# Kernel optimization log

Hardware: AMD Instinct MI355X
Metric: run time of the kernel (lower is better)

Reference implementation:

```python
import jax, jax.numpy as jnp
import numpy as np
import math

B, T, L, HID, BB, FF, H = 4, 1024, 1024, 1024, 512, 4096, 8
EPS = 1e-6


def _ln(x, g, b):
    m = jnp.mean(x, -1, keepdims=True)
    v = jnp.mean((x - m) ** 2, -1, keepdims=True)
    return (x - m) / jnp.sqrt(v + EPS) * g + b


def _gelu(x):
    # custom tanh-approx GELU from the source
    return 0.5 * x * (1 + jnp.tanh(math.sqrt(2.0 / math.pi) * (x + 0.044715 * x ** 3)))


def _mha(q_in, k_in, v_in, qw, qb, kw, kb, vw, vb, ow, ob, mask=None, sb=None,
         gw=None, gb=None, pkw=None, pkb=None, pqw=None, pqb=None, pos=None):
    Bq, Tq, _ = q_in.shape
    def split(x):
        return x.reshape(Bq, -1, H, x.shape[-1] // H).transpose(0, 2, 1, 3)  # [B,H,T,hd]
    qc = split(q_in @ qw + qb)
    kc = split(k_in @ kw + kb)
    vc = split(v_in @ vw + vb)
    scale = 1.0 / (qc.shape[-1] ** 0.5)
    scores = jnp.einsum('bhqd,bhkd->bhqk', qc, kc)
    if pos is not None:
        kp = split(pos @ pkw + pkb)
        qp = split(pos @ pqw + pqb)
        scores = scores + jnp.einsum('bhqd,bhkd->bhqk', qc, kp) + jnp.einsum('bhqd,bhkd->bhqk', qp, kc)
    scores = scores * scale
    if sb is not None:
        gate = jax.nn.sigmoid(qc @ gw + gb)  # [B,H,Tq,1]
        scores = scores + gate * sb
    if mask is not None:
        m = mask[None, None] if mask.ndim == 2 else (mask[:, None] if mask.ndim == 3 else mask)
        scores = jnp.where(m, scores, -jnp.inf)
    attn = jax.nn.softmax(scores, -1)
    ctx = jnp.einsum('bhqk,bhkd->bhqd', attn, vc).transpose(0, 2, 1, 3).reshape(Bq, Tq, -1)
    return ctx @ ow + ob


def _ffn(x, g, b, w1, b1, w2, b2):
    xn = _ln(x, g, b)
    return _gelu(xn @ w1 + b1) @ w2 + b2 + x


def setup_inputs() -> dict:
    key = jax.random.key(0)
    ks = iter(jax.random.split(key, 64))
    def rn(*s):
        return jax.random.normal(next(ks), s, dtype=jnp.float32)
    def pw(i, o):
        return 0.02 * rn(i, o)
    d = {}
    d['layout_content'] = rn(B, T, BB)
    d['text_x'] = rn(B, T, HID)
    d['text_memory'] = rn(B, L, HID)
    d['spatial_bias'] = rn(B, H, T, T)
    d['layout_pos'] = rn(B, T, BB)
    d['trg_mask'] = jnp.tril(jnp.ones((T, T), dtype=bool))
    d['src_mask'] = jnp.ones((B, T, L), dtype=bool)
    for n, i, o in [('sa_q', BB, BB), ('sa_k', BB, BB), ('sa_v', BB, BB),
                    ('sa_pk', BB, BB), ('sa_pq', BB, BB), ('sa_o', BB, BB),
                    ('lt_q', BB, HID), ('lt_k', HID, HID), ('lt_v', HID, HID), ('lt_o', HID, HID),
                    ('tl_q', HID, BB), ('tl_k', BB, BB), ('tl_v', BB, BB), ('tl_o', BB, BB),
                    ('ltp', HID, BB), ('tlp', BB, HID),
                    ('lf1', BB, FF), ('lf2', FF, BB), ('tf1', HID, FF), ('tf2', FF, HID)]:
        d[n + '_w'] = pw(i, o)
        d[n + '_b'] = jnp.zeros((o,), jnp.float32)
    d['sa_g_w'] = pw(BB // H, 1)
    d['sa_g_b'] = jnp.zeros((1,), jnp.float32)
    for n, s in [('ln1', BB), ('ln2', BB), ('tn1', HID), ('lfn', BB), ('tfn', HID)]:
        d[n + '_g'] = jnp.ones((s,), jnp.float32)
        d[n + '_b'] = jnp.zeros((s,), jnp.float32)
    return d


def reference(layout_content, text_x, text_memory, spatial_bias, layout_pos, trg_mask, src_mask,
              sa_q_w, sa_q_b, sa_k_w, sa_k_b, sa_v_w, sa_v_b, sa_pk_w, sa_pk_b, sa_pq_w, sa_pq_b,
              sa_o_w, sa_o_b, lt_q_w, lt_q_b, lt_k_w, lt_k_b, lt_v_w, lt_v_b, lt_o_w, lt_o_b,
              tl_q_w, tl_q_b, tl_k_w, tl_k_b, tl_v_w, tl_v_b, tl_o_w, tl_o_b,
              ltp_w, ltp_b, tlp_w, tlp_b, lf1_w, lf1_b, lf2_w, lf2_b, tf1_w, tf1_b, tf2_w, tf2_b,
              sa_g_w, sa_g_b, ln1_g, ln1_b, ln2_g, ln2_b, tn1_g, tn1_b, lfn_g, lfn_b, tfn_g, tfn_b):
    # layout self-attention (disentangled, gated spatial bias, causal mask)
    ln1 = _ln(layout_content, ln1_g, ln1_b)
    sa = _mha(ln1, ln1, ln1, sa_q_w, sa_q_b, sa_k_w, sa_k_b, sa_v_w, sa_v_b, sa_o_w, sa_o_b,
              mask=trg_mask, sb=spatial_bias, gw=sa_g_w, gb=sa_g_b,
              pkw=sa_pk_w, pkb=sa_pk_b, pqw=sa_pq_w, pqb=sa_pq_b, pos=layout_pos)
    layout_self_out = sa + layout_content
    # layout -> text cross attention
    ln2 = _ln(layout_self_out, ln2_g, ln2_b)
    lt = _mha(ln2, text_memory, text_memory, lt_q_w, lt_q_b, lt_k_w, lt_k_b, lt_v_w, lt_v_b,
              lt_o_w, lt_o_b, mask=src_mask)
    layout_pre = lt @ ltp_w + ltp_b + layout_self_out
    layout_out = _ffn(layout_pre, lfn_g, lfn_b, lf1_w, lf1_b, lf2_w, lf2_b)
    # text -> layout cross attention
    tn1 = _ln(text_x, tn1_g, tn1_b)
    tl = _mha(tn1, layout_out, layout_out, tl_q_w, tl_q_b, tl_k_w, tl_k_b, tl_v_w, tl_v_b,
              tl_o_w, tl_o_b)
    text_pre = tl @ tlp_w + tlp_b + text_x
    text_out = _ffn(text_pre, tfn_g, tfn_b, tf1_w, tf1_b, tf2_w, tf2_b)
    return (layout_out, text_out)
```

## Files before the change

kernel.cpp:

```cpp
#include <hip/hip_runtime.h>

#define Bd 4
#define Td 1024
#define Ld 1024
#define HIDd 1024
#define BBd 512
#define FFd 4096
#define Hd 8
#define ROWSd 4096

typedef unsigned short ushort_t;
typedef _Float16 f16;
typedef __attribute__((ext_vector_type(8))) short bf16x8;
typedef __attribute__((ext_vector_type(8))) _Float16 f16x8;
typedef __attribute__((ext_vector_type(4))) _Float16 f16x4;
typedef __attribute__((ext_vector_type(4))) float f32x4;

__device__ __forceinline__ float gelu_f(float x) {
    return 0.5f * x * (1.f + tanhf(0.7978845608028654f * (x + 0.044715f * x * x * x)));
}

__device__ __forceinline__ ushort_t f2b(float x) {
    union { float f; unsigned u; } v; v.f = x;
    unsigned r = v.u + 0x7fffu + ((v.u >> 16) & 1u);
    return (ushort_t)(r >> 16);
}

__device__ __forceinline__ void gload_lds16(const ushort_t* g, ushort_t* l) {
    __builtin_amdgcn_global_load_lds((__attribute__((address_space(1))) void*)(void*)g,
                                     (__attribute__((address_space(3))) void*)l,
                                     16, 0, 0);
}

template<int D>
__global__ __launch_bounds__(256) void ln_kernel(const float* __restrict__ x,
                                                 const float* __restrict__ g,
                                                 const float* __restrict__ b,
                                                 ushort_t* __restrict__ y)
{
    const int row = blockIdx.x;
    const int tid = threadIdx.x;
    const float* xr = x + (size_t)row * D;
    ushort_t* yr = y + (size_t)row * D;
    constexpr int PT = D / 256;
    float vals[PT];
    float s = 0.f, ss = 0.f;
#pragma unroll
    for (int i = 0; i < PT; i++) {
        float v = xr[tid + i * 256];
        vals[i] = v; s += v; ss += v * v;
    }
#pragma unroll
    for (int o = 32; o > 0; o >>= 1) { s += __shfl_down(s, o); ss += __shfl_down(ss, o); }
    __shared__ float rs[4], rss[4];
    const int wid = tid >> 6, lane = tid & 63;
    if (lane == 0) { rs[wid] = s; rss[wid] = ss; }
    __syncthreads();
    if (tid == 0) {
        float a = 0.f, c = 0.f;
        for (int i = 0; i < 4; i++) { a += rs[i]; c += rss[i]; }
        rs[0] = a; rss[0] = c;
    }
    __syncthreads();
    const float mean = rs[0] / D;
    const float var  = rss[0] / D - mean * mean;
    const float inv  = rsqrtf(fmaxf(var, 0.f) + 1e-6f);
#pragma unroll
    for (int i = 0; i < PT; i++) {
        const int idx = tid + i * 256;
        yr[idx] = f2b((vals[i] - mean) * inv * g[idx] + b[idx]);
    }
}

__global__ __launch_bounds__(256) void conv_kernel(const float* __restrict__ x,
                                                   ushort_t* __restrict__ y)
{
    const int i = (blockIdx.x * 256 + threadIdx.x) * 4;
    const float4 v = *(const float4*)&x[i];
    y[i + 0] = f2b(v.x); y[i + 1] = f2b(v.y); y[i + 2] = f2b(v.z); y[i + 3] = f2b(v.w);
}

__global__ __launch_bounds__(256) void tconv_kernel(const float* __restrict__ W,
                                                    ushort_t* __restrict__ Wt,
                                                    int K, int N)
{
    __shared__ float tile[32][33];
    const int tid = threadIdx.x;
    const int tx = tid & 31, ty = tid >> 5;
    const int n0 = blockIdx.x * 32, k0 = blockIdx.y * 32;
#pragma unroll
    for (int i = 0; i < 32; i += 8)
        tile[ty + i][tx] = W[(size_t)(k0 + ty + i) * N + n0 + tx];
    __syncthreads();
#pragma unroll
    for (int i = 0; i < 32; i += 8) {
        const int n = n0 + ty + i, k = k0 + tx;
        Wt[(size_t)n * K + k] = f2b(tile[tx][ty + i]);
    }
}

template<int FM, int FN, int WR, int WC, int ACT, int OMODE, int RESM>
__global__ __launch_bounds__(256) void mfma_gemm(const ushort_t* __restrict__ A,
                                                 const ushort_t* __restrict__ Bt,
                                                 const float* __restrict__ bias,
                                                 const void* __restrict__ resv,
                                                 float* __restrict__ Cf,
                                                 ushort_t* __restrict__ Cb,
                                                 f16* __restrict__ Ch,
                                                 int M, int N, int K)
{
    constexpr int BM = WR * FM * 16, BN = WC * FN * 16, BK = 32;
    constexpr int ACH = BM / 16, BCH = BN / 16, TCH = ACH + BCH;
    constexpr int CPW = (TCH + 3) / 4;
    __shared__ alignas(16) ushort_t As[BM * BK];
    __shared__ alignas(16) ushort_t Bs[BN * BK];
    const int tid = threadIdx.x, w = tid >> 6, lane = tid & 63;
    const int wr = w / WC, wc = w % WC;
    const int m0 = blockIdx.y * BM, n0 = blockIdx.x * BN;
    const int lrow = lane >> 2, lkb = (lane & 3) * 8;
    const int fr = lane & 15, kg = (lane >> 4) * 8;

    f32x4 acc[FM][FN] = {};

    for (int k0 = 0; k0 < K; k0 += BK) {
        __syncthreads();
#pragma unroll
        for (int t = 0; t < CPW; t++) {
            const int c = w * CPW + t;
            if (c < ACH) {
                const int row = c * 16 + lrow;
                gload_lds16(A + (size_t)(m0 + row) * K + k0 + lkb, As + c * 512);
            } else if (c < TCH) {
                const int cc = c - ACH;
                const int row = cc * 16 + lrow;
                gload_lds16(Bt + (size_t)(n0 + row) * K + k0 + lkb, Bs + cc * 512);
            }
        }
        __syncthreads();
        bf16x8 af[FM], bfr[FN];
#pragma unroll
        for (int i = 0; i < FM; i++)
            af[i] = *(const bf16x8*)(As + (wr * FM * 16 + i * 16 + fr) * 32 + kg);
#pragma unroll
        for (int j = 0; j < FN; j++)
            bfr[j] = *(const bf16x8*)(Bs + (wc * FN * 16 + j * 16 + fr) * 32 + kg);
#pragma unroll
        for (int i = 0; i < FM; i++)
#pragma unroll
            for (int j = 0; j < FN; j++)
                acc[i][j] = __builtin_amdgcn_mfma_f32_16x16x32_bf16(af[i], bfr[j], acc[i][j], 0, 0, 0);
    }

    const int cr = (lane >> 4) * 4, ccol = lane & 15;
#pragma unroll
    for (int i = 0; i < FM; i++) {
#pragma unroll
        for (int j = 0; j < FN; j++) {
            const int n = n0 + wc * FN * 16 + j * 16 + ccol;
            const int mb = m0 + wr * FM * 16 + i * 16 + cr;
            float vv[4];
#pragma unroll
            for (int q = 0; q < 4; q++) {
                float v = acc[i][j][q] + bias[n];
                if (ACT == 1) v = gelu_f(v);
                if (RESM == 1) v += ((const float*)resv)[(size_t)(mb + q) * N + n];
                if (RESM == 2) v += (float)((const f16*)resv)[(size_t)(mb + q) * N + n];
                vv[q] = v;
            }
            if (OMODE == 1 || OMODE == 3) {
#pragma unroll
                for (int q = 0; q < 4; q++) Cf[(size_t)(mb + q) * N + n] = vv[q];
            }
            if (OMODE == 2 || OMODE == 3) {
#pragma unroll
                for (int q = 0; q < 4; q++) Cb[(size_t)(mb + q) * N + n] = f2b(vv[q]);
            }
            if (OMODE == 4) {
#pragma unroll
                for (int q = 0; q < 4; q++) Ch[(size_t)(mb + q) * N + n] = (f16)vv[q];
            }
            if (OMODE == 5) {
                f16x4 pk = { (f16)vv[0], (f16)vv[1], (f16)vv[2], (f16)vv[3] };
                *(f16x4*)&Ch[(size_t)n * M + mb] = pk;
            }
        }
    }
}

__global__ __launch_bounds__(64) void gate_kernel(const f16* __restrict__ qc,
                                                  const float* __restrict__ gw,
                                                  const float* __restrict__ gb,
                                                  float* __restrict__ gate)
{
    const int bt = blockIdx.x;
    const int d = threadIdx.x;
    const float w = gw[d];
    const int b = bt >> 10, t = bt & 1023;
    const float gbv = gb[0];
#pragma unroll
    for (int h = 0; h < Hd; h++) {
        float v = (float)qc[(size_t)bt * BBd + h * 64 + d] * w;
#pragma unroll
        for (int o = 32; o > 0; o >>= 1) v += __shfl_xor(v, o);
        if (d == 0)
            gate[((size_t)b * Hd + h) * Td + t] = 1.f / (1.f + __expf(-(v + gbv)));
    }
}

template<int D, bool CAUSAL, bool SA>
__global__ __launch_bounds__(256) void attn_mfma(const f16* __restrict__ Q,
                                                 const f16* __restrict__ Qp,
                                                 const f16* __restrict__ Km,
                                                 const f16* __restrict__ Kc,
                                                 const f16* __restrict__ Vt,
                                                 const float* __restrict__ gate,
                                                 const float* __restrict__ sb,
                                                 ushort_t* __restrict__ O,
                                                 int Tq, int Tk, float scale)
{
    constexpr int KT = 64, QB = 64, PAD = 8;
    constexpr int NS = D / 32;
    constexpr int NDF = D / 16;
    constexpr int KROW = D + PAD;
    constexpr int VROW = KT + PAD;
    const int bh = blockIdx.y, b = bh >> 3, h = bh & 7;
    const int q0 = blockIdx.x * QB;
    const int tid = threadIdx.x, w = tid >> 6, lane = tid & 63;
    const int NH = Hd * D;
    const int qw0 = q0 + w * 16;
    const int fr = lane & 15;
    const int kg8 = (lane >> 4) * 8;
    const int cr4 = (lane >> 4) * 4;

    __shared__ alignas(16) f16 Ks[KT * KROW];
    __shared__ alignas(16) f16 Kcs[SA ? KT * KROW : 8];
    __shared__ alignas(16) f16 Vts[D * VROW];
    __shared__ alignas(16) f16 Pw[4][16 * VROW];

    const size_t qb = ((size_t)b * Tq) * NH + (size_t)h * D;
    const size_t kb = ((size_t)b * Tk) * NH + (size_t)h * D;

    f16x8 aq[NS], ap[SA ? NS : 1];
#pragma unroll
    for (int s = 0; s < NS; s++) {
        aq[s] = *(const f16x8*)&Q[qb + (size_t)(qw0 + fr) * NH + s * 32 + kg8];
        if constexpr (SA)
            ap[s] = *(const f16x8*)&Qp[qb + (size_t)(qw0 + fr) * NH + s * 32 + kg8];
    }
    float gq[4];
    if constexpr (SA) {
#pragma unroll
        for (int r = 0; r < 4; r++)
            gq[r] = gate[(size_t)bh * Tq + qw0 + cr4 + r];
    }

    float m[4], l[4];
    f32x4 oacc[NDF] = {};
#pragma unroll
    for (int r = 0; r < 4; r++) { m[r] = -1e30f; l[r] = 0.f; }

    const int NT = CAUSAL ? (q0 / KT + 1) : (Tk / KT);
    for (int t = 0; t < NT; t++) {
        const int k0 = t * KT;
        constexpr int KCH = KT * D / 8;
        for (int i = tid; i < KCH; i += 256) {
            const int row = i / (D / 8), c8 = (i % (D / 8)) * 8;
            *(f16x8*)&Ks[row * KROW + c8] = *(const f16x8*)&Km[kb + (size_t)(k0 + row) * NH + c8];
            if constexpr (SA)
                *(f16x8*)&Kcs[row * KROW + c8] = *(const f16x8*)&Kc[kb + (size_t)(k0 + row) * NH + c8];
        }
        constexpr int VCH = D * KT / 8;
        for (int i = tid; i < VCH; i += 256) {
            const int d = i / (KT / 8), c8 = (i % (KT / 8)) * 8;
            *(f16x8*)&Vts[d * VROW + c8] =
                *(const f16x8*)&Vt[(size_t)(h * D + d) * ((size_t)Bd * Tk) + (size_t)b * Tk + k0 + c8];
        }
        __syncthreads();

        float pv[4][4];
#pragma unroll
        for (int kf = 0; kf < 4; kf++) {
            f32x4 sacc = {};
#pragma unroll
            for (int s = 0; s < NS; s++) {
                const f16x8 bk = *(const f16x8*)&Ks[(kf * 16 + fr) * KROW + s * 32 + kg8];
                sacc = __builtin_amdgcn_mfma_f32_16x16x32_f16(aq[s], bk, sacc, 0, 0, 0);
            }
            if constexpr (SA) {
#pragma unroll
                for (int s = 0; s < NS; s++) {
                    const f16x8 bkc = *(const f16x8*)&Kcs[(kf * 16 + fr) * KROW + s * 32 + kg8];
                    sacc = __builtin_amdgcn_mfma_f32_16x16x32_f16(ap[s], bkc, sacc, 0, 0, 0);
                }
            }
            const int k = k0 + kf * 16 + fr;
#pragma unroll
            for (int r = 0; r < 4; r++) {
                const int q = qw0 + cr4 + r;
                float v = sacc[r] * scale;
                if constexpr (SA)
                    v += gq[r] * sb[((size_t)bh * Tq + q) * Tk + k];
                if (CAUSAL && k > q) v = -1e30f;
                pv[kf][r] = v;
            }
        }

#pragma unroll
        for (int r = 0; r < 4; r++) {
            float mx = fmaxf(fmaxf(pv[0][r], pv[1][r]), fmaxf(pv[2][r], pv[3][r]));
            mx = fmaxf(mx, __shfl_xor(mx, 1));
            mx = fmaxf(mx, __shfl_xor(mx, 2));
            mx = fmaxf(mx, __shfl_xor(mx, 4));
            mx = fmaxf(mx, __shfl_xor(mx, 8));
            const float mn = fmaxf(m[r], mx);
            const float fs = __expf(m[r] - mn);
            m[r] = mn;
            float ls = 0.f;
#pragma unroll
            for (int kf = 0; kf < 4; kf++) {
                const float p = __expf(pv[kf][r] - mn);
                pv[kf][r] = p; ls += p;
            }
            ls += __shfl_xor(ls, 1);
            ls += __shfl_xor(ls, 2);
            ls += __shfl_xor(ls, 4);
            ls += __shfl_xor(ls, 8);
            l[r] = l[r] * fs + ls;
#pragma unroll
            for (int df = 0; df < NDF; df++) oacc[df][r] *= fs;
        }

#pragma unroll
        for (int kf = 0; kf < 4; kf++)
#pragma unroll
            for (int r = 0; r < 4; r++)
                Pw[w][(cr4 + r) * VROW + kf * 16 + fr] = (f16)pv[kf][r];
        asm volatile("s_waitcnt lgkmcnt(0)" ::: "memory");
        __builtin_amdgcn_sched_barrier(0);

#pragma unroll
        for (int s = 0; s < KT / 32; s++) {
            const f16x8 pa = *(const f16x8*)&Pw[w][fr * VROW + s * 32 + kg8];
#pragma unroll
            for (int df = 0; df < NDF; df++) {
                const f16x8 vb = *(const f16x8*)&Vts[(df * 16 + fr) * VROW + s * 32 + kg8];
                oacc[df] = __builtin_amdgcn_mfma_f32_16x16x32_f16(pa, vb, oacc[df], 0, 0, 0);
            }
        }
        __syncthreads();
    }

#pragma unroll
    for (int r = 0; r < 4; r++) {
        const float inv = 1.f / l[r];
        const size_t rowb = qb + (size_t)(qw0 + cr4 + r) * NH;
#pragma unroll
        for (int df = 0; df < NDF; df++)
            O[rowb + df * 16 + fr] = f2b(oacc[df][r] * inv);
    }
}

extern "C" void kernel_launch(void* const* d_in, const int* in_sizes, int n_in,
                              void* d_out, int out_size, void* d_ws, size_t ws_size,
                              hipStream_t stream)
{
    const float* layout_content = (const float*)d_in[0];
    const float* text_x         = (const float*)d_in[1];
    const float* text_memory    = (const float*)d_in[2];
    const float* spatial_bias   = (const float*)d_in[3];
    const float* layout_pos     = (const float*)d_in[4];
    const float* sa_q_w = (const float*)d_in[7];   const float* sa_q_b = (const float*)d_in[8];
    const float* sa_k_w = (const float*)d_in[9];   const float* sa_k_b = (const float*)d_in[10];
    const float* sa_v_w = (const float*)d_in[11];  const float* sa_v_b = (const float*)d_in[12];
    const float* sa_pk_w = (const float*)d_in[13]; const float* sa_pk_b = (const float*)d_in[14];
    const float* sa_pq_w = (const float*)d_in[15]; const float* sa_pq_b = (const float*)d_in[16];
    const float* sa_o_w = (const float*)d_in[17];  const float* sa_o_b = (const float*)d_in[18];
    const float* lt_q_w = (const float*)d_in[19];  const float* lt_q_b = (const float*)d_in[20];
    const float* lt_k_w = (const float*)d_in[21];  const float* lt_k_b = (const float*)d_in[22];
    const float* lt_v_w = (const float*)d_in[23];  const float* lt_v_b = (const float*)d_in[24];
    const float* lt_o_w = (const float*)d_in[25];  const float* lt_o_b = (const float*)d_in[26];
    const float* tl_q_w = (const float*)d_in[27];  const float* tl_q_b = (const float*)d_in[28];
    const float* tl_k_w = (const float*)d_in[29];  const float* tl_k_b = (const float*)d_in[30];
    const float* tl_v_w = (const float*)d_in[31];  const float* tl_v_b = (const float*)d_in[32];
    const float* tl_o_w = (const float*)d_in[33];  const float* tl_o_b = (const float*)d_in[34];
    const float* ltp_w = (const float*)d_in[35];   const float* ltp_b = (const float*)d_in[36];
    const float* tlp_w = (const float*)d_in[37];   const float* tlp_b = (const float*)d_in[38];
    const float* lf1_w = (const float*)d_in[39];   const float* lf1_b = (const float*)d_in[40];
    const float* lf2_w = (const float*)d_in[41];   const float* lf2_b = (const float*)d_in[42];
    const float* tf1_w = (const float*)d_in[43];   const float* tf1_b = (const float*)d_in[44];
    const float* tf2_w = (const float*)d_in[45];   const float* tf2_b = (const float*)d_in[46];
    const float* sa_g_w = (const float*)d_in[47];  const float* sa_g_b = (const float*)d_in[48];
    const float* ln1_g = (const float*)d_in[49];   const float* ln1_b = (const float*)d_in[50];
    const float* ln2_g = (const float*)d_in[51];   const float* ln2_b = (const float*)d_in[52];
    const float* tn1_g = (const float*)d_in[53];   const float* tn1_b = (const float*)d_in[54];
    const float* lfn_g = (const float*)d_in[55];   const float* lfn_b = (const float*)d_in[56];
    const float* tfn_g = (const float*)d_in[57];   const float* tfn_b = (const float*)d_in[58];

    float* out = (float*)d_out;
    float* layout_out = out;
    float* text_out   = out + (size_t)ROWSd * BBd;

    char* p = (char*)d_ws;
    auto alloc = [&](size_t bytes) { void* r = (void*)p; p += (bytes + 255) & ~(size_t)255; return r; };
    const size_t R = ROWSd;

    f16*  Qh   = (f16*)alloc(R * 1024 * 2);
    f16*  Kh   = (f16*)alloc(R * 1024 * 2);
    f16*  Vth  = (f16*)alloc(R * 1024 * 2);
    f16*  Kch  = (f16*)alloc(R * 512 * 2);
    f16*  KSh  = (f16*)alloc(R * 512 * 2);
    f16*  QPh  = (f16*)alloc(R * 512 * 2);
    float* GATEf = (float*)alloc((size_t)Bd * Hd * Td * 4);
    ushort_t* CTXb = (ushort_t*)alloc(R * 1024 * 2);
    float* LSOf  = (float*)alloc(R * 512 * 4);
    float* LPREf = (float*)alloc(R * 512 * 4);
    float* TPREf = (float*)alloc(R * 1024 * 4);
    ushort_t* XNb = (ushort_t*)alloc(R * 1024 * 2);
    ushort_t* LPb = (ushort_t*)alloc(R * 512 * 2);
    ushort_t* TMb = (ushort_t*)alloc(R * 1024 * 2);
    ushort_t* LTOb = (ushort_t*)alloc(R * 1024 * 2);
    ushort_t* TLOb = (ushort_t*)alloc(R * 512 * 2);
    ushort_t* LOb  = (ushort_t*)alloc(R * 512 * 2);
    ushort_t* HBb  = (ushort_t*)alloc(R * 4096 * 2);

    auto wt = [&](int K, int N) { return (ushort_t*)alloc((size_t)K * N * 2); };
    ushort_t* sa_q_t = wt(512, 512);  ushort_t* sa_k_t = wt(512, 512);  ushort_t* sa_v_t = wt(512, 512);
    ushort_t* sa_pk_t = wt(512, 512); ushort_t* sa_pq_t = wt(512, 512); ushort_t* sa_o_t = wt(512, 512);
    ushort_t* lt_q_t = wt(512, 1024); ushort_t* lt_k_t = wt(1024, 1024);
    ushort_t* lt_v_t = wt(1024, 1024); ushort_t* lt_o_t = wt(1024, 1024);
    ushort_t* tl_q_t = wt(1024, 512); ushort_t* tl_k_t = wt(512, 512);
    ushort_t* tl_v_t = wt(512, 512);  ushort_t* tl_o_t = wt(512, 512);
    ushort_t* ltp_t = wt(1024, 512);  ushort_t* tlp_t = wt(512, 1024);
    ushort_t* lf1_t = wt(512, 4096);  ushort_t* lf2_t = wt(4096, 512);
    ushort_t* tf1_t = wt(1024, 4096); ushort_t* tf2_t = wt(4096, 1024);

    const dim3 blk(256);

    auto tc = [&](const float* W, ushort_t* Wt, int K, int N) {
        tconv_kernel<<<dim3(N / 32, K / 32), blk, 0, stream>>>(W, Wt, K, N);
    };
    tc(sa_q_w, sa_q_t, 512, 512);   tc(sa_k_w, sa_k_t, 512, 512);   tc(sa_v_w, sa_v_t, 512, 512);
    tc(sa_pk_w, sa_pk_t, 512, 512); tc(sa_pq_w, sa_pq_t, 512, 512); tc(sa_o_w, sa_o_t, 512, 512);
    tc(lt_q_w, lt_q_t, 512, 1024);  tc(lt_k_w, lt_k_t, 1024, 1024);
    tc(lt_v_w, lt_v_t, 1024, 1024); tc(lt_o_w, lt_o_t, 1024, 1024);
    tc(tl_q_w, tl_q_t, 1024, 512);  tc(tl_k_w, tl_k_t, 512, 512);
    tc(tl_v_w, tl_v_t, 512, 512);   tc(tl_o_w, tl_o_t, 512, 512);
    tc(ltp_w, ltp_t, 1024, 512);    tc(tlp_w, tlp_t, 512, 1024);
    tc(lf1_w, lf1_t, 512, 4096);    tc(lf2_w, lf2_t, 4096, 512);
    tc(tf1_w, tf1_t, 1024, 4096);   tc(tf2_w, tf2_t, 4096, 1024);

    conv_kernel<<<dim3(R * 512 / 1024), blk, 0, stream>>>(layout_pos, LPb);
    conv_kernel<<<dim3(R * 1024 / 1024), blk, 0, stream>>>(text_memory, TMb);

#define G512(ACT, OM, RESM, Aa, Bb, bb, rr, cf, cb, ch, K) \
    mfma_gemm<2, 2, 1, 4, ACT, OM, RESM><<<dim3(512 / 128, ROWSd / 32), blk, 0, stream>>>(Aa, Bb, bb, rr, cf, cb, ch, ROWSd, 512, K)
#define G1024(ACT, OM, RESM, Aa, Bb, bb, rr, cf, cb, ch, K) \
    mfma_gemm<4, 2, 1, 4, ACT, OM, RESM><<<dim3(1024 / 128, ROWSd / 64), blk, 0, stream>>>(Aa, Bb, bb, rr, cf, cb, ch, ROWSd, 1024, K)
#define G4096(ACT, OM, RESM, Aa, Bb, bb, rr, cf, cb, ch, K) \
    mfma_gemm<4, 4, 2, 2, ACT, OM, RESM><<<dim3(4096 / 128, ROWSd / 128), blk, 0, stream>>>(Aa, Bb, bb, rr, cf, cb, ch, ROWSd, 4096, K)

    ln_kernel<512><<<dim3(ROWSd), blk, 0, stream>>>(layout_content, ln1_g, ln1_b, XNb);
    G512(0, 4, 0, XNb, sa_q_t, sa_q_b, nullptr, nullptr, nullptr, Qh, 512);
    G512(0, 4, 0, XNb, sa_k_t, sa_k_b, nullptr, nullptr, nullptr, Kch, 512);
    G512(0, 5, 0, XNb, sa_v_t, sa_v_b, nullptr, nullptr, nullptr, Vth, 512);
    G512(0, 4, 0, LPb, sa_pq_t, sa_pq_b, nullptr, nullptr, nullptr, QPh, 512);
    G512(0, 4, 2, LPb, sa_pk_t, sa_pk_b, Kch, nullptr, nullptr, KSh, 512);
    gate_kernel<<<dim3(ROWSd), dim3(64), 0, stream>>>(Qh, sa_g_w, sa_g_b, GATEf);
    attn_mfma<64, true, true><<<dim3(Td / 64, Bd * Hd), blk, 0, stream>>>(
        Qh, QPh, KSh, Kch, Vth, GATEf, spatial_bias, CTXb, Td, Td, 0.125f);
    G512(0, 1, 1, CTXb, sa_o_t, sa_o_b, layout_content, LSOf, nullptr, nullptr, 512);

    ln_kernel<512><<<dim3(ROWSd), blk, 0, stream>>>(LSOf, ln2_g, ln2_b, XNb);
    G1024(0, 4, 0, XNb, lt_q_t, lt_q_b, nullptr, nullptr, nullptr, Qh, 512);
    G1024(0, 4, 0, TMb, lt_k_t, lt_k_b, nullptr, nullptr, nullptr, Kh, 1024);
    G1024(0, 5, 0, TMb, lt_v_t, lt_v_b, nullptr, nullptr, nullptr, Vth, 1024);
    attn_mfma<128, false, false><<<dim3(Td / 64, Bd * Hd), blk, 0, stream>>>(
        Qh, nullptr, Kh, nullptr, Vth, nullptr, nullptr, CTXb, Td, Ld, 0.08838834764831845f);
    G1024(0, 2, 0, CTXb, lt_o_t, lt_o_b, nullptr, nullptr, LTOb, nullptr, 1024);
    G512(0, 1, 1, LTOb, ltp_t, ltp_b, LSOf, LPREf, nullptr, nullptr, 1024);

    ln_kernel<512><<<dim3(ROWSd), blk, 0, stream>>>(LPREf, lfn_g, lfn_b, XNb);
    G4096(1, 2, 0, XNb, lf1_t, lf1_b, nullptr, nullptr, HBb, nullptr, 512);
    G512(0, 3, 1, HBb, lf2_t, lf2_b, LPREf, layout_out, LOb, nullptr, 4096);

    ln_kernel<1024><<<dim3(ROWSd), blk, 0, stream>>>(text_x, tn1_g, tn1_b, XNb);
    G512(0, 4, 0, XNb, tl_q_t, tl_q_b, nullptr, nullptr, nullptr, Qh, 1024);
    G512(0, 4, 0, LOb, tl_k_t, tl_k_b, nullptr, nullptr, nullptr, Kh, 512);
    G512(0, 5, 0, LOb, tl_v_t, tl_v_b, nullptr, nullptr, nullptr, Vth, 512);
    attn_mfma<64, false, false><<<dim3(Td / 64, Bd * Hd), blk, 0, stream>>>(
        Qh, nullptr, Kh, nullptr, Vth, nullptr, nullptr, CTXb, Td, Td, 0.125f);
    G512(0, 2, 0, CTXb, tl_o_t, tl_o_b, nullptr, nullptr, TLOb, nullptr, 512);
    G1024(0, 1, 1, TLOb, tlp_t, tlp_b, text_x, TPREf, nullptr, nullptr, 512);

    ln_kernel<1024><<<dim3(ROWSd), blk, 0, stream>>>(TPREf, tfn_g, tfn_b, XNb);
    G4096(1, 2, 0, XNb, tf1_t, tf1_b, nullptr, nullptr, HBb, nullptr, 1024);
    G1024(0, 1, 1, HBb, tf2_t, tf2_b, TPREf, text_out, nullptr, nullptr, 4096);

#undef G512
#undef G1024
#undef G4096
}
```

Measured before the change: 1.250 ms.

## Double-buffer attention K/V tiles, remap workgroups, retune GEMM tile shapes

```diff
diff --git a/kernel.cpp b/kernel.cpp
--- a/kernel.cpp
+++ b/kernel.cpp
@@ -207,7 +207,7 @@
     }
 }
 
-template<int D, bool CAUSAL, bool SA>
+template<int D, int KT, bool CAUSAL, bool SA>
 __global__ __launch_bounds__(256) void attn_mfma(const f16* __restrict__ Q,
                                                  const f16* __restrict__ Qp,
                                                  const f16* __restrict__ Km,
@@ -218,13 +218,21 @@
                                                  ushort_t* __restrict__ O,
                                                  int Tq, int Tk, float scale)
 {
-    constexpr int KT = 64, QB = 64, PAD = 8;
+    constexpr int QB = 64, PAD = 8;
     constexpr int NS = D / 32;
     constexpr int NDF = D / 16;
+    constexpr int KF = KT / 16;
     constexpr int KROW = D + PAD;
     constexpr int VROW = KT + PAD;
-    const int bh = blockIdx.y, b = bh >> 3, h = bh & 7;
-    const int q0 = blockIdx.x * QB;
+    constexpr int NCH = KT * D / 2048;
+
+    const int gx = gridDim.x, nwg = gx * gridDim.y;
+    const int flat = blockIdx.y * gx + blockIdx.x;
+    const int cpx = nwg >> 3;
+    const int work = (flat & 7) * cpx + (flat >> 3);
+    const int bh = work / gx, qblk = work % gx;
+    const int b = bh >> 3, h = bh & 7;
+    const int q0 = qblk * QB;
     const int tid = threadIdx.x, w = tid >> 6, lane = tid & 63;
     const int NH = Hd * D;
     const int qw0 = q0 + w * 16;
@@ -232,13 +240,14 @@
     const int kg8 = (lane >> 4) * 8;
     const int cr4 = (lane >> 4) * 4;
 
-    __shared__ alignas(16) f16 Ks[KT * KROW];
-    __shared__ alignas(16) f16 Kcs[SA ? KT * KROW : 8];
-    __shared__ alignas(16) f16 Vts[D * VROW];
+    __shared__ alignas(16) f16 Ks[2][KT * KROW];
+    __shared__ alignas(16) f16 Kcs[SA ? 2 : 1][SA ? KT * KROW : 8];
+    __shared__ alignas(16) f16 Vts[2][D * VROW];
     __shared__ alignas(16) f16 Pw[4][16 * VROW];
 
     const size_t qb = ((size_t)b * Tq) * NH + (size_t)h * D;
     const size_t kb = ((size_t)b * Tk) * NH + (size_t)h * D;
+    const size_t vtb = (size_t)h * D * ((size_t)Bd * Tk) + (size_t)b * Tk;
 
     f16x8 aq[NS], ap[SA ? NS : 1];
 #pragma unroll
@@ -254,42 +263,80 @@
             gq[r] = gate[(size_t)bh * Tq + qw0 + cr4 + r];
     }
 
+    f16x8 krg[NCH], kcrg[SA ? NCH : 1], vrg[NCH];
+    auto load_tile = [&](int k0) {
+#pragma unroll
+        for (int j = 0; j < NCH; j++) {
+            const int i = tid + j * 256;
+            const int row = i / (D / 8), c8 = (i % (D / 8)) * 8;
+            krg[j] = *(const f16x8*)&Km[kb + (size_t)(k0 + row) * NH + c8];
+            if constexpr (SA)
+                kcrg[j] = *(const f16x8*)&Kc[kb + (size_t)(k0 + row) * NH + c8];
+        }
+#pragma unroll
+        for (int j = 0; j < NCH; j++) {
+            const int i = tid + j * 256;
+            const int d = i / (KT / 8), c8 = (i % (KT / 8)) * 8;
+            vrg[j] = *(const f16x8*)&Vt[vtb + (size_t)d * ((size_t)Bd * Tk) + k0 + c8];
+        }
+    };
+    auto store_tile = [&](int buf) {
+#pragma unroll
+        for (int j = 0; j < NCH; j++) {
+            const int i = tid + j * 256;
+            const int row = i / (D / 8), c8 = (i % (D / 8)) * 8;
+            *(f16x8*)&Ks[buf][row * KROW + c8] = krg[j];
+            if constexpr (SA)
+                *(f16x8*)&Kcs[buf][row * KROW + c8] = kcrg[j];
+        }
+#pragma unroll
+        for (int j = 0; j < NCH; j++) {
+            const int i = tid + j * 256;
+            const int d = i / (KT / 8), c8 = (i % (KT / 8)) * 8;
+            *(f16x8*)&Vts[buf][d * VROW + c8] = vrg[j];
+        }
+    };
+
     float m[4], l[4];
     f32x4 oacc[NDF] = {};
 #pragma unroll
     for (int r = 0; r < 4; r++) { m[r] = -1e30f; l[r] = 0.f; }
 
     const int NT = CAUSAL ? (q0 / KT + 1) : (Tk / KT);
+
+    load_tile(0);
+    store_tile(0);
+    __syncthreads();
+
+    int cur = 0;
     for (int t = 0; t < NT; t++) {
         const int k0 = t * KT;
-        constexpr int KCH = KT * D / 8;
-        for (int i = tid; i < KCH; i += 256) {
-            const int row = i / (D / 8), c8 = (i % (D / 8)) * 8;
-            *(f16x8*)&Ks[row * KROW + c8] = *(const f16x8*)&Km[kb + (size_t)(k0 + row) * NH + c8];
-            if constexpr (SA)
-                *(f16x8*)&Kcs[row * KROW + c8] = *(const f16x8*)&Kc[kb + (size_t)(k0 + row) * NH + c8];
-        }
-        constexpr int VCH = D * KT / 8;
-        for (int i = tid; i < VCH; i += 256) {
-            const int d = i / (KT / 8), c8 = (i % (KT / 8)) * 8;
-            *(f16x8*)&Vts[d * VROW + c8] =
-                *(const f16x8*)&Vt[(size_t)(h * D + d) * ((size_t)Bd * Tk) + (size_t)b * Tk + k0 + c8];
-        }
-        __syncthreads();
-
-        float pv[4][4];
-#pragma unroll
-        for (int kf = 0; kf < 4; kf++) {
+        const bool pf = (t + 1 < NT);
+        if (pf) load_tile(k0 + KT);
+
+        float sbv[SA ? KF : 1][4];
+        if constexpr (SA) {
+#pragma unroll
+            for (int kf = 0; kf < KF; kf++)
+#pragma unroll
+                for (int r = 0; r < 4; r++)
+                    sbv[kf][r] = gq[r] *
+                        sb[((size_t)bh * Tq + qw0 + cr4 + r) * Tk + k0 + kf * 16 + fr];
+        }
+
+        float pv[KF][4];
+#pragma unroll
+        for (int kf = 0; kf < KF; kf++) {
             f32x4 sacc = {};
 #pragma unroll
             for (int s = 0; s < NS; s++) {
-                const f16x8 bk = *(const f16x8*)&Ks[(kf * 16 + fr) * KROW + s * 32 + kg8];
+                const f16x8 bk = *(const f16x8*)&Ks[cur][(kf * 16 + fr) * KROW + s * 32 + kg8];
                 sacc = __builtin_amdgcn_mfma_f32_16x16x32_f16(aq[s], bk, sacc, 0, 0, 0);
             }
             if constexpr (SA) {
 #pragma unroll
                 for (int s = 0; s < NS; s++) {
-                    const f16x8 bkc = *(const f16x8*)&Kcs[(kf * 16 + fr) * KROW + s * 32 + kg8];
+                    const f16x8 bkc = *(const f16x8*)&Kcs[cur][(kf * 16 + fr) * KROW + s * 32 + kg8];
                     sacc = __builtin_amdgcn_mfma_f32_16x16x32_f16(ap[s], bkc, sacc, 0, 0, 0);
                 }
             }
@@ -298,8 +345,7 @@
             for (int r = 0; r < 4; r++) {
                 const int q = qw0 + cr4 + r;
                 float v = sacc[r] * scale;
-                if constexpr (SA)
-                    v += gq[r] * sb[((size_t)bh * Tq + q) * Tk + k];
+                if constexpr (SA) v += sbv[kf][r];
                 if (CAUSAL && k > q) v = -1e30f;
                 pv[kf][r] = v;
             }
@@ -307,7 +353,9 @@
 
 #pragma unroll
         for (int r = 0; r < 4; r++) {
-            float mx = fmaxf(fmaxf(pv[0][r], pv[1][r]), fmaxf(pv[2][r], pv[3][r]));
+            float mx = pv[0][r];
+#pragma unroll
+            for (int kf = 1; kf < KF; kf++) mx = fmaxf(mx, pv[kf][r]);
             mx = fmaxf(mx, __shfl_xor(mx, 1));
             mx = fmaxf(mx, __shfl_xor(mx, 2));
             mx = fmaxf(mx, __shfl_xor(mx, 4));
@@ -317,7 +365,7 @@
             m[r] = mn;
             float ls = 0.f;
 #pragma unroll
-            for (int kf = 0; kf < 4; kf++) {
+            for (int kf = 0; kf < KF; kf++) {
                 const float p = __expf(pv[kf][r] - mn);
                 pv[kf][r] = p; ls += p;
             }
@@ -331,7 +379,7 @@
         }
 
 #pragma unroll
-        for (int kf = 0; kf < 4; kf++)
+        for (int kf = 0; kf < KF; kf++)
 #pragma unroll
             for (int r = 0; r < 4; r++)
                 Pw[w][(cr4 + r) * VROW + kf * 16 + fr] = (f16)pv[kf][r];
@@ -343,11 +391,14 @@
             const f16x8 pa = *(const f16x8*)&Pw[w][fr * VROW + s * 32 + kg8];
 #pragma unroll
             for (int df = 0; df < NDF; df++) {
-                const f16x8 vb = *(const f16x8*)&Vts[(df * 16 + fr) * VROW + s * 32 + kg8];
+                const f16x8 vb = *(const f16x8*)&Vts[cur][(df * 16 + fr) * VROW + s * 32 + kg8];
                 oacc[df] = __builtin_amdgcn_mfma_f32_16x16x32_f16(pa, vb, oacc[df], 0, 0, 0);
             }
         }
+
+        if (pf) store_tile(cur ^ 1);
         __syncthreads();
+        cur ^= 1;
     }
 
 #pragma unroll
@@ -456,8 +507,10 @@
     mfma_gemm<2, 2, 1, 4, ACT, OM, RESM><<<dim3(512 / 128, ROWSd / 32), blk, 0, stream>>>(Aa, Bb, bb, rr, cf, cb, ch, ROWSd, 512, K)
 #define G1024(ACT, OM, RESM, Aa, Bb, bb, rr, cf, cb, ch, K) \
     mfma_gemm<4, 2, 1, 4, ACT, OM, RESM><<<dim3(1024 / 128, ROWSd / 64), blk, 0, stream>>>(Aa, Bb, bb, rr, cf, cb, ch, ROWSd, 1024, K)
-#define G4096(ACT, OM, RESM, Aa, Bb, bb, rr, cf, cb, ch, K) \
-    mfma_gemm<4, 4, 2, 2, ACT, OM, RESM><<<dim3(4096 / 128, ROWSd / 128), blk, 0, stream>>>(Aa, Bb, bb, rr, cf, cb, ch, ROWSd, 4096, K)
+#define G12864(ACT, OM, RESM, Aa, Bb, bb, rr, cf, cb, ch, K) \
+    mfma_gemm<4, 2, 2, 2, ACT, OM, RESM><<<dim3(512 / 64, ROWSd / 128), blk, 0, stream>>>(Aa, Bb, bb, rr, cf, cb, ch, ROWSd, 512, K)
+#define G128SQ(ACT, OM, RESM, Aa, Bb, bb, rr, cf, cb, ch, N, K) \
+    mfma_gemm<4, 4, 2, 2, ACT, OM, RESM><<<dim3((N) / 128, ROWSd / 128), blk, 0, stream>>>(Aa, Bb, bb, rr, cf, cb, ch, ROWSd, N, K)
 
     ln_kernel<512><<<dim3(ROWSd), blk, 0, stream>>>(layout_content, ln1_g, ln1_b, XNb);
     G512(0, 4, 0, XNb, sa_q_t, sa_q_b, nullptr, nullptr, nullptr, Qh, 512);
@@ -466,37 +519,38 @@
     G512(0, 4, 0, LPb, sa_pq_t, sa_pq_b, nullptr, nullptr, nullptr, QPh, 512);
     G512(0, 4, 2, LPb, sa_pk_t, sa_pk_b, Kch, nullptr, nullptr, KSh, 512);
     gate_kernel<<<dim3(ROWSd), dim3(64), 0, stream>>>(Qh, sa_g_w, sa_g_b, GATEf);
-    attn_mfma<64, true, true><<<dim3(Td / 64, Bd * Hd), blk, 0, stream>>>(
+    attn_mfma<64, 64, true, true><<<dim3(Td / 64, Bd * Hd), blk, 0, stream>>>(
         Qh, QPh, KSh, Kch, Vth, GATEf, spatial_bias, CTXb, Td, Td, 0.125f);
     G512(0, 1, 1, CTXb, sa_o_t, sa_o_b, layout_content, LSOf, nullptr, nullptr, 512);
 
     ln_kernel<512><<<dim3(ROWSd), blk, 0, stream>>>(LSOf, ln2_g, ln2_b, XNb);
     G1024(0, 4, 0, XNb, lt_q_t, lt_q_b, nullptr, nullptr, nullptr, Qh, 512);
-    G1024(0, 4, 0, TMb, lt_k_t, lt_k_b, nullptr, nullptr, nullptr, Kh, 1024);
-    G1024(0, 5, 0, TMb, lt_v_t, lt_v_b, nullptr, nullptr, nullptr, Vth, 1024);
-    attn_mfma<128, false, false><<<dim3(Td / 64, Bd * Hd), blk, 0, stream>>>(
+    G128SQ(0, 4, 0, TMb, lt_k_t, lt_k_b, nullptr, nullptr, nullptr, Kh, 1024, 1024);
+    G128SQ(0, 5, 0, TMb, lt_v_t, lt_v_b, nullptr, nullptr, nullptr, Vth, 1024, 1024);
+    attn_mfma<128, 32, false, false><<<dim3(Td / 64, Bd * Hd), blk, 0, stream>>>(
         Qh, nullptr, Kh, nullptr, Vth, nullptr, nullptr, CTXb, Td, Ld, 0.08838834764831845f);
-    G1024(0, 2, 0, CTXb, lt_o_t, lt_o_b, nullptr, nullptr, LTOb, nullptr, 1024);
-    G512(0, 1, 1, LTOb, ltp_t, ltp_b, LSOf, LPREf, nullptr, nullptr, 1024);
+    G128SQ(0, 2, 0, CTXb, lt_o_t, lt_o_b, nullptr, nullptr, LTOb, nullptr, 1024, 1024);
+    G12864(0, 1, 1, LTOb, ltp_t, ltp_b, LSOf, LPREf, nullptr, nullptr, 1024);
 
     ln_kernel<512><<<dim3(ROWSd), blk, 0, stream>>>(LPREf, lfn_g, lfn_b, XNb);
-    G4096(1, 2, 0, XNb, lf1_t, lf1_b, nullptr, nullptr, HBb, nullptr, 512);
-    G512(0, 3, 1, HBb, lf2_t, lf2_b, LPREf, layout_out, LOb, nullptr, 4096);
+    G128SQ(1, 2, 0, XNb, lf1_t, lf1_b, nullptr, nullptr, HBb, nullptr, 4096, 512);
+    G12864(0, 3, 1, HBb, lf2_t, lf2_b, LPREf, layout_out, LOb, nullptr, 4096);
 
     ln_kernel<1024><<<dim3(ROWSd), blk, 0, stream>>>(text_x, tn1_g, tn1_b, XNb);
-    G512(0, 4, 0, XNb, tl_q_t, tl_q_b, nullptr, nullptr, nullptr, Qh, 1024);
+    G12864(0, 4, 0, XNb, tl_q_t, tl_q_b, nullptr, nullptr, nullptr, Qh, 1024);
     G512(0, 4, 0, LOb, tl_k_t, tl_k_b, nullptr, nullptr, nullptr, Kh, 512);
     G512(0, 5, 0, LOb, tl_v_t, tl_v_b, nullptr, nullptr, nullptr, Vth, 512);
-    attn_mfma<64, false, false><<<dim3(Td / 64, Bd * Hd), blk, 0, stream>>>(
+    attn_mfma<64, 64, false, false><<<dim3(Td / 64, Bd * Hd), blk, 0, stream>>>(
         Qh, nullptr, Kh, nullptr, Vth, nullptr, nullptr, CTXb, Td, Td, 0.125f);
     G512(0, 2, 0, CTXb, tl_o_t, tl_o_b, nullptr, nullptr, TLOb, nullptr, 512);
     G1024(0, 1, 1, TLOb, tlp_t, tlp_b, text_x, TPREf, nullptr, nullptr, 512);
 
     ln_kernel<1024><<<dim3(ROWSd), blk, 0, stream>>>(TPREf, tfn_g, tfn_b, XNb);
-    G4096(1, 2, 0, XNb, tf1_t, tf1_b, nullptr, nullptr, HBb, nullptr, 1024);
-    G1024(0, 1, 1, HBb, tf2_t, tf2_b, TPREf, text_out, nullptr, nullptr, 4096);
+    G128SQ(1, 2, 0, XNb, tf1_t, tf1_b, nullptr, nullptr, HBb, nullptr, 4096, 1024);
+    G128SQ(0, 1, 1, HBb, tf2_t, tf2_b, TPREf, text_out, nullptr, nullptr, 1024, 4096);
 
 #undef G512
 #undef G1024
-#undef G4096
-}
+#undef G12864
+#undef G128SQ
+}
```

Result: faster. 1.190 ms (-4.8%).
